# Kernel optimization log

Hardware: AMD Instinct MI355X
Metric: run time of the kernel (lower is better)

## Reference

```python
import jax, jax.numpy as jnp
import numpy as np
from jax import lax

NUM_HEADS = 8
RATIO_H = 2
RATIO_W = 2


def _layer_norm(x, gamma, beta, eps=1e-5):
    mean = jnp.mean(x, axis=-1, keepdims=True)
    var = jnp.var(x, axis=-1, keepdims=True)
    return (x - mean) * lax.rsqrt(var + eps) * gamma + beta


def setup_inputs() -> dict:
    key = jax.random.key(0)
    ks = jax.random.split(key, 6)
    B, N, C = 4, 4096, 512
    std = 0.02
    return {
        "x": jax.random.normal(ks[0], (B, N, C), jnp.float32),
        "w_qkv": jax.random.normal(ks[1], (3 * C, C), jnp.float32) * std,
        "w_ke": jax.random.normal(ks[2], (C, C, RATIO_H, RATIO_W), jnp.float32) * std,
        "w_ve": jax.random.normal(ks[3], (C, C, RATIO_H, RATIO_W), jnp.float32) * std,
        "gamma_k": jnp.ones((C // NUM_HEADS,), jnp.float32),
        "beta_k": jnp.zeros((C // NUM_HEADS,), jnp.float32),
        "gamma_v": jnp.ones((C // NUM_HEADS,), jnp.float32),
        "beta_v": jnp.zeros((C // NUM_HEADS,), jnp.float32),
        "w_proj": jax.random.normal(ks[4], (C, C), jnp.float32) * std,
        "b_proj": jnp.zeros((C,), jnp.float32),
    }


def reference(x, w_qkv, w_ke, w_ve, gamma_k, beta_k, gamma_v, beta_v, w_proj, b_proj):
    B, N, C = x.shape
    H = W = int(np.sqrt(N))
    h = NUM_HEADS
    hd = C // h
    s = RATIO_H * RATIO_W
    scale = hd ** -0.5

    # qkv projection (no bias): [B, N, 3C]
    qkv = jnp.einsum('bnc,dc->bnd', x, w_qkv)
    q, k, v = jnp.split(qkv, 3, axis=-1)

    # q -> [B, h, N, hd]
    q = q.reshape(B, N, h, hd).transpose(0, 2, 1, 3)

    # spatial reduction of k, v via strided conv (kernel == stride, no bias)
    def reduce_kv(t, w):
        img = t.transpose(0, 2, 1).reshape(B, C, H, W)
        red = lax.conv_general_dilated(
            img, w, window_strides=(RATIO_H, RATIO_W), padding='VALID',
            dimension_numbers=('NCHW', 'OIHW', 'NCHW'))  # [B, C, H/rh, W/rw]
        return red.reshape(B, C, N // s).transpose(0, 2, 1).reshape(
            B, N // s, h, hd).transpose(0, 2, 1, 3)  # [B, h, N/s, hd]

    k = _layer_norm(reduce_kv(k, w_ke), gamma_k, beta_k)
    v = _layer_norm(reduce_kv(v, w_ve), gamma_v, beta_v)

    # attention: [B, h, N, N/s]
    attn = jax.nn.softmax(jnp.einsum('bhqd,bhkd->bhqk', q, k) * scale, axis=-1)
    out = jnp.einsum('bhqk,bhkd->bhqd', attn, v)  # [B, h, N, hd]
    out = out.transpose(0, 2, 1, 3).reshape(B, N, C)
    return jnp.einsum('bnc,dc->bnd', out, w_proj) + b_proj
```

## Files before the change

### kernel.cpp

```cpp
#include <hip/hip_runtime.h>
#include <hip/hip_bf16.h>

#define DEVI static __device__ __forceinline__

typedef __attribute__((ext_vector_type(4))) float f32x4;
typedef __attribute__((ext_vector_type(8))) short bf16x8;
typedef __attribute__((ext_vector_type(4))) short s16x4;
typedef __attribute__((ext_vector_type(2))) unsigned int u32x2;

DEVI unsigned short f2bf(float f) {
    union { float f; unsigned u; } v; v.f = f;
    unsigned r = v.u + 0x7fffu + ((v.u >> 16) & 1u);
    return (unsigned short)(r >> 16);
}

DEVI void gload_lds16(const void* g, void* l) {
    __builtin_amdgcn_global_load_lds(
        (const __attribute__((address_space(1))) unsigned int*)(g),
        (__attribute__((address_space(3))) unsigned int*)(l), 16, 0, 0);
}

#define EXP2A(d, x) asm("v_exp_f32 %0, %1" : "=v"(d) : "v"(x))
#define CVTPK(d, a, b) asm("v_cvt_pk_bf16_f32 %0, %1, %2" : "=v"(d) : "v"(a), "v"(b))

__global__ __launch_bounds__(256) void prep_kernel(
    const float* __restrict__ x, const float* __restrict__ w_qkv,
    const float* __restrict__ w_proj, const float* __restrict__ w_ke,
    const float* __restrict__ w_ve,
    unsigned short* __restrict__ xb, unsigned short* __restrict__ wqkvb,
    unsigned short* __restrict__ wprojb, unsigned short* __restrict__ w2k,
    unsigned short* __restrict__ w2v, unsigned short* __restrict__ wqkvT)
{
    const int blk = blockIdx.x, t = threadIdx.x;
    if (blk < 9216) {
        const float* src; unsigned short* dst; int i;
        if (blk < 8192)      { src = x;      dst = xb;     i = (blk * 256 + t) * 4; }
        else if (blk < 8960) { src = w_qkv;  dst = wqkvb;  i = ((blk - 8192) * 256 + t) * 4; }
        else                 { src = w_proj; dst = wprojb; i = ((blk - 8960) * 256 + t) * 4; }
        const float4 v = *(const float4*)(src + i);
        ushort4 o; o.x = f2bf(v.x); o.y = f2bf(v.y); o.z = f2bf(v.z); o.w = f2bf(v.w);
        *(ushort4*)(dst + i) = o;
    } else if (blk < 11264) {
        const int r = blk - 9216;
        const float* wsrc = (r < 1024) ? w_ke : w_ve;
        unsigned short* wdst = (r < 1024) ? w2k : w2v;
        const int i4 = (((r & 1023) * 256) + t) * 4;
        const int o = i4 >> 11, p = (i4 >> 9) & 3, c = i4 & 511;
        const float* s = wsrc + (o << 11) + (c << 2) + p;
        ushort4 ov; ov.x = f2bf(s[0]); ov.y = f2bf(s[4]); ov.z = f2bf(s[8]); ov.w = f2bf(s[12]);
        *(ushort4*)(wdst + i4) = ov;
    } else {
        const int r2 = blk - 11264;
        const int i4 = (r2 * 256 + t) * 4;
        const int sel = i4 >> 18;
        const int rem = i4 & 262143;
        const int d = rem >> 9, c4 = rem & 511;
        const float* s = w_qkv + (size_t)(512 + sel * 512 + c4) * 512 + d;
        ushort4 ov; ov.x = f2bf(s[0]); ov.y = f2bf(s[512]); ov.z = f2bf(s[1024]); ov.w = f2bf(s[1536]);
        *(ushort4*)(wqkvT + i4) = ov;
    }
}

template<int OUT_BF16, int ADD_BIAS>
__global__ __launch_bounds__(256) void gemm_bt(
    const unsigned short* __restrict__ A,
    const unsigned short* __restrict__ B,
    void* __restrict__ Cp, const float* __restrict__ bias,
    int N, int K)
{
    __shared__ unsigned short As[128 * 64];
    __shared__ unsigned short Bs[128 * 64];
    const int t = threadIdx.x;
    const int lane = t & 63, w = t >> 6;
    const int wr = w >> 1, wc = w & 1;
    const int lr = lane & 15, lg = lane >> 4;
    const size_t rowBase = (size_t)blockIdx.y * 128;
    const size_t colBase = (size_t)blockIdx.x * 128;

    const unsigned short* gA[4]; const unsigned short* gB[4]; int du[4];
#pragma unroll
    for (int j = 0; j < 4; ++j) {
        const int u = t * 16 + j * 4096;
        const int row = u >> 7, colb = u & 127;
        const int csw = colb ^ ((row & 7) << 4);
        du[j] = u;
        gA[j] = A + (rowBase + row) * (size_t)K + (csw >> 1);
        gB[j] = B + (colBase + row) * (size_t)K + (csw >> 1);
    }
    const int sw = (lr & 7) << 4;

    f32x4 acc[4][4] = {};

    for (int k0 = 0; k0 < K; k0 += 64) {
#pragma unroll
        for (int j = 0; j < 4; ++j) {
            gload_lds16(gA[j] + k0, (char*)As + du[j]);
            gload_lds16(gB[j] + k0, (char*)Bs + du[j]);
        }
        __syncthreads();
#pragma unroll
        for (int s = 0; s < 2; ++s) {
            const int ro = (s * 64 + lg * 16) ^ sw;
            bf16x8 af[4], bfr[4];
#pragma unroll
            for (int a = 0; a < 4; ++a)
                af[a] = *(const bf16x8*)((char*)As + (wr * 64 + a * 16 + lr) * 128 + ro);
#pragma unroll
            for (int bn = 0; bn < 4; ++bn)
                bfr[bn] = *(const bf16x8*)((char*)Bs + (wc * 64 + bn * 16 + lr) * 128 + ro);
#pragma unroll
            for (int a = 0; a < 4; ++a)
#pragma unroll
                for (int bn = 0; bn < 4; ++bn)
                    acc[a][bn] = __builtin_amdgcn_mfma_f32_16x16x32_bf16(af[a], bfr[bn], acc[a][bn], 0, 0, 0);
        }
        __syncthreads();
    }

#pragma unroll
    for (int a = 0; a < 4; ++a) {
        const size_t row = rowBase + wr * 64 + a * 16 + lg * 4;
#pragma unroll
        for (int bn = 0; bn < 4; ++bn) {
            const size_t col = colBase + wc * 64 + bn * 16 + lr;
#pragma unroll
            for (int r = 0; r < 4; ++r) {
                const float v = acc[a][bn][r];
                if (OUT_BF16) {
                    ((unsigned short*)Cp)[(row + r) * (size_t)N + col] = f2bf(v);
                } else {
                    const float vb2 = ADD_BIAS ? (v + bias[col]) : v;
                    ((float*)Cp)[(row + r) * (size_t)N + col] = vb2;
                }
            }
        }
    }
}

__global__ __launch_bounds__(256) void gemm_wt(
    const unsigned short* __restrict__ w2k,
    const unsigned short* __restrict__ w2v,
    const unsigned short* __restrict__ wqkvT,
    unsigned short* __restrict__ wtk,
    unsigned short* __restrict__ wtv)
{
    __shared__ unsigned short As[128 * 64];
    __shared__ unsigned short Bs[128 * 64];
    const int t = threadIdx.x;
    const int lane = t & 63, w = t >> 6;
    const int wr = w >> 1, wc = w & 1;
    const int lr = lane & 15, lg = lane >> 4;
    const int rowBase = blockIdx.y * 128;
    const int colBase = blockIdx.x * 128;
    const int p = blockIdx.z & 3, sel = blockIdx.z >> 2;
    const unsigned short* A = (sel ? w2v : w2k) + p * 512;
    const unsigned short* B = wqkvT + (size_t)sel * 262144;
    unsigned short* C = (sel ? wtv : wtk) + p * 512;

    const unsigned short* gA[4]; const unsigned short* gB[4]; int du[4];
#pragma unroll
    for (int j = 0; j < 4; ++j) {
        const int u = t * 16 + j * 4096;
        const int row = u >> 7, colb = u & 127;
        const int csw = colb ^ ((row & 7) << 4);
        du[j] = u;
        gA[j] = A + (size_t)(rowBase + row) * 2048 + (csw >> 1);
        gB[j] = B + (size_t)(colBase + row) * 512 + (csw >> 1);
    }
    const int sw = (lr & 7) << 4;

    f32x4 acc[4][4] = {};

    for (int k0 = 0; k0 < 512; k0 += 64) {
#pragma unroll
        for (int j = 0; j < 4; ++j) {
            gload_lds16(gA[j] + k0, (char*)As + du[j]);
            gload_lds16(gB[j] + k0, (char*)Bs + du[j]);
        }
        __syncthreads();
#pragma unroll
        for (int s = 0; s < 2; ++s) {
            const int ro = (s * 64 + lg * 16) ^ sw;
            bf16x8 af[4], bfr[4];
#pragma unroll
            for (int a = 0; a < 4; ++a)
                af[a] = *(const bf16x8*)((char*)As + (wr * 64 + a * 16 + lr) * 128 + ro);
#pragma unroll
            for (int bn = 0; bn < 4; ++bn)
                bfr[bn] = *(const bf16x8*)((char*)Bs + (wc * 64 + bn * 16 + lr) * 128 + ro);
#pragma unroll
            for (int a = 0; a < 4; ++a)
#pragma unroll
                for (int bn = 0; bn < 4; ++bn)
                    acc[a][bn] = __builtin_amdgcn_mfma_f32_16x16x32_bf16(af[a], bfr[bn], acc[a][bn], 0, 0, 0);
        }
        __syncthreads();
    }

#pragma unroll
    for (int a = 0; a < 4; ++a) {
        const size_t row = (size_t)rowBase + wr * 64 + a * 16 + lg * 4;
#pragma unroll
        for (int bn = 0; bn < 4; ++bn) {
            const size_t col = (size_t)colBase + wc * 64 + bn * 16 + lr;
#pragma unroll
            for (int r = 0; r < 4; ++r)
                C[(row + r) * 2048 + col] = f2bf(acc[a][bn][r]);
        }
    }
}

__global__ __launch_bounds__(256) void gemm_red(
    const unsigned short* __restrict__ xb,
    const unsigned short* __restrict__ wtk,
    const unsigned short* __restrict__ wtv,
    float* __restrict__ kred)
{
    __shared__ unsigned short As[128 * 64];
    __shared__ unsigned short Bs[128 * 64];
    const int t = threadIdx.x;
    const int lane = t & 63, w = t >> 6;
    const int wr = w >> 1, wc = w & 1;
    const int lr = lane & 15, lg = lane >> 4;
    const int rowBase = blockIdx.y * 128;
    const int colBase = blockIdx.x * 128;
    const int ks = blockIdx.z;
    const int isV = rowBase >= 4096;
    const unsigned short* Bp = isV ? wtv : wtk;

    const char* gA[4]; const unsigned short* gB[4]; int du[4];
#pragma unroll
    for (int j = 0; j < 4; ++j) {
        const int u = t * 16 + j * 4096;
        const int row = u >> 7, colb = u & 127;
        const int csw = colb ^ ((row & 7) << 4);
        du[j] = u;
        const int bm = (rowBase + row) & 4095;
        const int b = bm >> 10, m = bm & 1023;
        const int pix = (m >> 5) * 128 + (m & 31) * 2;
        gA[j] = (const char*)xb + (size_t)(b * 4096 + pix) * 1024 + csw;
        gB[j] = Bp + (colBase + row) * (size_t)2048 + (csw >> 1);
    }
    const int sw = (lr & 7) << 4;

    f32x4 acc[4][4] = {};

    for (int kk = 0; kk < 16; ++kk) {
        const int k0 = ks * 1024 + kk * 64;
        const int p = k0 >> 9;
        const int pd = ((p & 1) ? 1 : 0) + ((p & 2) ? 64 : 0);
        const size_t aoff = (size_t)pd * 1024 + (size_t)(k0 & 511) * 2;
#pragma unroll
        for (int j = 0; j < 4; ++j) {
            gload_lds16(gA[j] + aoff, (char*)As + du[j]);
            gload_lds16(gB[j] + k0, (char*)Bs + du[j]);
        }
        __syncthreads();
#pragma unroll
        for (int s = 0; s < 2; ++s) {
            const int ro = (s * 64 + lg * 16) ^ sw;
            bf16x8 af[4], bfr[4];
#pragma unroll
            for (int a = 0; a < 4; ++a)
                af[a] = *(const bf16x8*)((char*)As + (wr * 64 + a * 16 + lr) * 128 + ro);
#pragma unroll
            for (int bn = 0; bn < 4; ++bn)
                bfr[bn] = *(const bf16x8*)((char*)Bs + (wc * 64 + bn * 16 + lr) * 128 + ro);
#pragma unroll
            for (int a = 0; a < 4; ++a)
#pragma unroll
                for (int bn = 0; bn < 4; ++bn)
                    acc[a][bn] = __builtin_amdgcn_mfma_f32_16x16x32_bf16(af[a], bfr[bn], acc[a][bn], 0, 0, 0);
        }
        __syncthreads();
    }

    float* outp = kred + (size_t)ks * 4194304;
#pragma unroll
    for (int a = 0; a < 4; ++a) {
        const size_t row = (size_t)rowBase + wr * 64 + a * 16 + lg * 4;
#pragma unroll
        for (int bn = 0; bn < 4; ++bn) {
            const size_t col = (size_t)colBase + wc * 64 + bn * 16 + lr;
#pragma unroll
            for (int r = 0; r < 4; ++r)
                outp[(row + r) * 512 + col] = acc[a][bn][r];
        }
    }
}

__global__ __launch_bounds__(256) void ln_kernel(
    const float* __restrict__ kredA, const float* __restrict__ kredB,
    const float* __restrict__ gk, const float* __restrict__ bk,
    const float* __restrict__ gv, const float* __restrict__ bv,
    unsigned short* __restrict__ outp)
{
    const int bm = blockIdx.x;
    const int sel = blockIdx.y;
    const size_t off = ((size_t)sel * 4096 + bm) * 512;
    const float* g = sel ? gv : gk;
    const float* be = sel ? bv : bk;
    const float QS = sel ? 1.0f : 0.18033688011112042f;
    unsigned short* o = outp + off;
    const int t = threadIdx.x;
    const float2 a = *(const float2*)(kredA + off + t * 2);
    const float2 b2 = *(const float2*)(kredB + off + t * 2);
    const float vx = a.x + b2.x, vy = a.y + b2.y;
    float s = vx + vy, s2 = vx * vx + vy * vy;
#pragma unroll
    for (int o2 = 1; o2 <= 16; o2 <<= 1) {
        s += __shfl_xor(s, o2);
        s2 += __shfl_xor(s2, o2);
    }
    const float mean = s * 0.015625f;
    const float var = s2 * 0.015625f - mean * mean;
    const float rstd = rsqrtf(var + 1e-5f);
    const int c = (t * 2) & 63;
    ushort2 ov;
    ov.x = f2bf(((vx - mean) * rstd * g[c] + be[c]) * QS);
    ov.y = f2bf(((vy - mean) * rstd * g[c + 1] + be[c + 1]) * QS);
    *(ushort2*)(o + t * 2) = ov;
}

__global__ __launch_bounds__(256) void transpose_v(
    const unsigned short* __restrict__ v_ln, unsigned short* __restrict__ v_t)
{
    __shared__ unsigned short tile[64][65];
    const int mb = blockIdx.x;
    const int cb = blockIdx.y;
    const int t = threadIdx.x;
#pragma unroll
    for (int i = 0; i < 16; ++i) {
        const int idx = i * 256 + t;
        const int r = idx >> 6, c = idx & 63;
        tile[r][c] = v_ln[(size_t)(mb * 64 + r) * 512 + cb * 64 + c];
    }
    __syncthreads();
    const int b = mb >> 4;
    const int mloc = (mb & 15) * 64;
#pragma unroll
    for (int i = 0; i < 16; ++i) {
        const int idx = i * 256 + t;
        const int c = idx >> 6, m = idx & 63;
        v_t[((size_t)(b * 512) + cb * 64 + c) * 1024 + mloc + m] = tile[m][c];
    }
}

__global__ __launch_bounds__(256) void attn_kernel(
    const unsigned short* __restrict__ qb,
    const unsigned short* __restrict__ k_ln,
    const unsigned short* __restrict__ v_t,
    unsigned short* __restrict__ attn_out)
{
    extern __shared__ char smem[];
    const int blk = ((blockIdx.x & 7) << 7) | (blockIdx.x >> 3);
    const int qc = blk & 31, h = (blk >> 5) & 7, b = blk >> 8;
    const int t = threadIdx.x, w = t >> 6, lane = t & 63;
    const int lr = lane & 15, lg = lane >> 4;
    const int qrow0 = qc * 128 + w * 32;

    const unsigned short* qpA = qb + (size_t)(b * 4096 + qrow0 + lr) * 512 + h * 64 + lg * 8;
    const bf16x8 qa0 = *(const bf16x8*)(qpA);
    const bf16x8 qa1 = *(const bf16x8*)(qpA + 32);
    const bf16x8 qb0 = *(const bf16x8*)(qpA + 16 * 512);
    const bf16x8 qb1 = *(const bf16x8*)(qpA + 16 * 512 + 32);

    const char* kbase = (const char*)(k_ln + (size_t)b * 524288 + h * 64);
    const char* vbase = (const char*)(v_t + ((size_t)b * 512 + h * 64) * 1024);
    const int d0 = t * 16, d1 = 4096 + t * 16;
    const int r0 = d0 >> 7, cs0 = (d0 & 127) ^ ((r0 & 7) << 4);
    const int r1 = d1 >> 7, cs1 = (d1 & 127) ^ ((r1 & 7) << 4);
    const char* gK0 = kbase + r0 * 1024 + cs0;
    const char* gK1 = kbase + r1 * 1024 + cs1;
    const char* gV0 = vbase + r0 * 2048 + cs0;
    const char* gV1 = vbase + r1 * 2048 + cs1;

#define STAGE_KV(buf, kt) do { \
    gload_lds16(gK0 + (size_t)(kt) * 65536, smem + (buf) * 8192 + d0); \
    gload_lds16(gK1 + (size_t)(kt) * 65536, smem + (buf) * 8192 + d1); \
    gload_lds16(gV0 + (kt) * 128, smem + 16384 + (buf) * 8192 + d0); \
    gload_lds16(gV1 + (kt) * 128, smem + 16384 + (buf) * 8192 + d1); \
  } while (0)

    bf16x8 ones;
#pragma unroll
    for (int i = 0; i < 8; ++i) ones[i] = (short)0x3F80;

    f32x4 accA[4] = {}, accB[4] = {};
    f32x4 psaccA = {}, psaccB = {};

    STAGE_KV(0, 0);
    __syncthreads();

    char* Pw = smem + 32768 + w * 2048;
    const int sw = (lr & 7) << 4;
    const int off0 = lr * 128 + ((lg * 16) ^ sw);
    const int off1 = lr * 128 + ((64 + lg * 16) ^ sw);
    int pwo[4];
#pragma unroll
    for (int tt = 0; tt < 4; ++tt) pwo[tt] = lr * 128 + ((tt * 32 + lg * 8) ^ sw);

#pragma unroll 2
    for (int kt = 0; kt < 16; ++kt) {
        const int cur = kt & 1;
        if (kt < 15) STAGE_KV(cur ^ 1, kt + 1);
        const char* KsB = smem + cur * 8192;
        const char* VsB = smem + 16384 + cur * 8192;

        f32x4 sa[4], sb[4];
#pragma unroll
        for (int tt = 0; tt < 4; ++tt) {
            const bf16x8 kf0 = *(const bf16x8*)(KsB + tt * 2048 + off0);
            const bf16x8 kf1 = *(const bf16x8*)(KsB + tt * 2048 + off1);
            f32x4 za = {}, zb = {};
            za = __builtin_amdgcn_mfma_f32_16x16x32_bf16(kf0, qa0, za, 0, 0, 0);
            za = __builtin_amdgcn_mfma_f32_16x16x32_bf16(kf1, qa1, za, 0, 0, 0);
            zb = __builtin_amdgcn_mfma_f32_16x16x32_bf16(kf0, qb0, zb, 0, 0, 0);
            zb = __builtin_amdgcn_mfma_f32_16x16x32_bf16(kf1, qb1, zb, 0, 0, 0);
            sa[tt] = za; sb[tt] = zb;
        }

#pragma unroll
        for (int tt = 0; tt < 4; ++tt) {
            float e0, e1, e2, e3;
            EXP2A(e0, sa[tt][0]); EXP2A(e1, sa[tt][1]);
            EXP2A(e2, sa[tt][2]); EXP2A(e3, sa[tt][3]);
            unsigned c0, c1;
            CVTPK(c0, e0, e1); CVTPK(c1, e2, e3);
            union { u32x2 u; s16x4 s; } pk; pk.u.x = c0; pk.u.y = c1;
            *(s16x4*)(Pw + pwo[tt]) = pk.s;
        }
        asm volatile("" ::: "memory");
        const bf16x8 fa0 = *(const bf16x8*)(Pw + off0);
        const bf16x8 fa1 = *(const bf16x8*)(Pw + off1);
        asm volatile("" ::: "memory");

        bf16x8 vf0[4], vf1[4];
#pragma unroll
        for (int n2 = 0; n2 < 4; ++n2) {
            vf0[n2] = *(const bf16x8*)(VsB + n2 * 2048 + off0);
            vf1[n2] = *(const bf16x8*)(VsB + n2 * 2048 + off1);
        }

#pragma unroll
        for (int n2 = 0; n2 < 4; ++n2) {
            accA[n2] = __builtin_amdgcn_mfma_f32_16x16x32_bf16(fa0, vf0[n2], accA[n2], 0, 0, 0);
            accA[n2] = __builtin_amdgcn_mfma_f32_16x16x32_bf16(fa1, vf1[n2], accA[n2], 0, 0, 0);
        }
        psaccA = __builtin_amdgcn_mfma_f32_16x16x32_bf16(fa0, ones, psaccA, 0, 0, 0);
        psaccA = __builtin_amdgcn_mfma_f32_16x16x32_bf16(fa1, ones, psaccA, 0, 0, 0);

#pragma unroll
        for (int tt = 0; tt < 4; ++tt) {
            float e0, e1, e2, e3;
            EXP2A(e0, sb[tt][0]); EXP2A(e1, sb[tt][1]);
            EXP2A(e2, sb[tt][2]); EXP2A(e3, sb[tt][3]);
            unsigned c0, c1;
            CVTPK(c0, e0, e1); CVTPK(c1, e2, e3);
            union { u32x2 u; s16x4 s; } pk; pk.u.x = c0; pk.u.y = c1;
            *(s16x4*)(Pw + pwo[tt]) = pk.s;
        }
        asm volatile("" ::: "memory");
        const bf16x8 fb0 = *(const bf16x8*)(Pw + off0);
        const bf16x8 fb1 = *(const bf16x8*)(Pw + off1);

#pragma unroll
        for (int n2 = 0; n2 < 4; ++n2) {
            accB[n2] = __builtin_amdgcn_mfma_f32_16x16x32_bf16(fb0, vf0[n2], accB[n2], 0, 0, 0);
            accB[n2] = __builtin_amdgcn_mfma_f32_16x16x32_bf16(fb1, vf1[n2], accB[n2], 0, 0, 0);
        }
        psaccB = __builtin_amdgcn_mfma_f32_16x16x32_bf16(fb0, ones, psaccB, 0, 0, 0);
        psaccB = __builtin_amdgcn_mfma_f32_16x16x32_bf16(fb1, ones, psaccB, 0, 0, 0);
        __syncthreads();
    }
#undef STAGE_KV

    float dA[4], dB[4];
#pragma unroll
    for (int r = 0; r < 4; ++r) {
        dA[r] = 1.0f / psaccA[r];
        dB[r] = 1.0f / psaccB[r];
    }
    unsigned short* oA = attn_out + (size_t)(b * 4096 + qrow0 + lg * 4) * 512 + h * 64;
#pragma unroll
    for (int n2 = 0; n2 < 4; ++n2)
#pragma unroll
        for (int r = 0; r < 4; ++r) {
            oA[(size_t)r * 512 + n2 * 16 + lr] = f2bf(accA[n2][r] * dA[r]);
            oA[(size_t)(16 + r) * 512 + n2 * 16 + lr] = f2bf(accB[n2][r] * dB[r]);
        }
}

extern "C" void kernel_launch(void* const* d_in, const int* in_sizes, int n_in,
                              void* d_out, int out_size, void* d_ws, size_t ws_size,
                              hipStream_t stream)
{
    (void)in_sizes; (void)n_in; (void)out_size; (void)ws_size;
    const float* x       = (const float*)d_in[0];
    const float* w_qkv   = (const float*)d_in[1];
    const float* w_ke    = (const float*)d_in[2];
    const float* w_ve    = (const float*)d_in[3];
    const float* gamma_k = (const float*)d_in[4];
    const float* beta_k  = (const float*)d_in[5];
    const float* gamma_v = (const float*)d_in[6];
    const float* beta_v  = (const float*)d_in[7];
    const float* w_proj  = (const float*)d_in[8];
    const float* b_proj  = (const float*)d_in[9];
    float* out = (float*)d_out;

    char* ws = (char*)d_ws;
    unsigned short* qb     = (unsigned short*)(ws + 0);
    unsigned short* wtk    = (unsigned short*)(ws + 16777216);
    unsigned short* wtv    = (unsigned short*)(ws + 18874368);
    unsigned short* wqkvT  = (unsigned short*)(ws + 20971520);
    unsigned short* xb     = (unsigned short*)(ws + 50331648);
    unsigned short* attn_o = xb;
    float*          kredB  = (float*)(ws + 67108864);
    float*          kredA  = (float*)(ws + 83886080);
    unsigned short* k_ln   = (unsigned short*)(ws + 100663296);
    unsigned short* v_ln   = (unsigned short*)(ws + 104857600);
    unsigned short* v_t    = (unsigned short*)(ws + 109051904);
    unsigned short* wqkvb  = (unsigned short*)(ws + 113246208);
    unsigned short* w2k    = (unsigned short*)(ws + 114819072);
    unsigned short* w2v    = (unsigned short*)(ws + 116916224);
    unsigned short* wprojb = (unsigned short*)(ws + 119013376);

    prep_kernel<<<11776, 256, 0, stream>>>(x, w_qkv, w_proj, w_ke, w_ve,
                                           xb, wqkvb, wprojb, w2k, w2v, wqkvT);

    gemm_wt<<<dim3(4, 4, 8), 256, 0, stream>>>(w2k, w2v, wqkvT, wtk, wtv);

    gemm_bt<1, 0><<<dim3(4, 128), 256, 0, stream>>>(
        xb, wqkvb, qb, nullptr, 512, 512);

    gemm_red<<<dim3(4, 64, 2), 256, 0, stream>>>(xb, wtk, wtv, kredB);

    ln_kernel<<<dim3(4096, 2), 256, 0, stream>>>(kredA, kredB,
                                                 gamma_k, beta_k, gamma_v, beta_v, k_ln);

    transpose_v<<<dim3(64, 8), 256, 0, stream>>>(v_ln, v_t);

    attn_kernel<<<1024, 256, 40960, stream>>>(qb, k_ln, v_t, attn_o);

    gemm_bt<0, 1><<<dim3(4, 128), 256, 0, stream>>>(
        attn_o, wprojb, out, b_proj, 512, 512);
}
```

Measured before the change: 145.4 us.

## Merge Q projection and KV reduction GEMMs into one launch; prioritize MFMA in attention

Combines the Q projection GEMM and the spatial-reduction K/V GEMM into a single kernel launch whose grid is split by blockIdx.y, so both workloads share the GPU concurrently and one launch plus its tail is removed. Also wraps the MFMA sections of the attention loop with s_setprio raising wave priority, to favor matrix-core issue over exp/convert phases of other waves. The merged kernel carries both code paths, which may raise register usage and lower occupancy.

```diff
diff --git a/kernel.cpp b/kernel.cpp
--- a/kernel.cpp
+++ b/kernel.cpp
@@ -210,8 +210,10 @@
     }
 }
 
-__global__ __launch_bounds__(256) void gemm_red(
+__global__ __launch_bounds__(256) void gemm_qred(
     const unsigned short* __restrict__ xb,
+    const unsigned short* __restrict__ wqkvb,
+    unsigned short* __restrict__ qbuf,
     const unsigned short* __restrict__ wtk,
     const unsigned short* __restrict__ wtv,
     float* __restrict__ kred)
@@ -222,69 +224,119 @@
     const int lane = t & 63, w = t >> 6;
     const int wr = w >> 1, wc = w & 1;
     const int lr = lane & 15, lg = lane >> 4;
-    const int rowBase = blockIdx.y * 128;
+    const int sw = (lr & 7) << 4;
     const int colBase = blockIdx.x * 128;
-    const int ks = blockIdx.z;
-    const int isV = rowBase >= 4096;
-    const unsigned short* Bp = isV ? wtv : wtk;
-
-    const char* gA[4]; const unsigned short* gB[4]; int du[4];
-#pragma unroll
-    for (int j = 0; j < 4; ++j) {
-        const int u = t * 16 + j * 4096;
-        const int row = u >> 7, colb = u & 127;
-        const int csw = colb ^ ((row & 7) << 4);
-        du[j] = u;
-        const int bm = (rowBase + row) & 4095;
-        const int b = bm >> 10, m = bm & 1023;
-        const int pix = (m >> 5) * 128 + (m & 31) * 2;
-        gA[j] = (const char*)xb + (size_t)(b * 4096 + pix) * 1024 + csw;
-        gB[j] = Bp + (colBase + row) * (size_t)2048 + (csw >> 1);
-    }
-    const int sw = (lr & 7) << 4;
-
-    f32x4 acc[4][4] = {};
-
-    for (int kk = 0; kk < 16; ++kk) {
-        const int k0 = ks * 1024 + kk * 64;
-        const int p = k0 >> 9;
-        const int pd = ((p & 1) ? 1 : 0) + ((p & 2) ? 64 : 0);
-        const size_t aoff = (size_t)pd * 1024 + (size_t)(k0 & 511) * 2;
+
+    if (blockIdx.y < 128) {
+        const size_t rowBase = (size_t)blockIdx.y * 128;
+        const unsigned short* gA[4]; const unsigned short* gB[4]; int du[4];
 #pragma unroll
         for (int j = 0; j < 4; ++j) {
-            gload_lds16(gA[j] + aoff, (char*)As + du[j]);
-            gload_lds16(gB[j] + k0, (char*)Bs + du[j]);
-        }
-        __syncthreads();
-#pragma unroll
-        for (int s = 0; s < 2; ++s) {
-            const int ro = (s * 64 + lg * 16) ^ sw;
-            bf16x8 af[4], bfr[4];
-#pragma unroll
-            for (int a = 0; a < 4; ++a)
-                af[a] = *(const bf16x8*)((char*)As + (wr * 64 + a * 16 + lr) * 128 + ro);
-#pragma unroll
-            for (int bn = 0; bn < 4; ++bn)
-                bfr[bn] = *(const bf16x8*)((char*)Bs + (wc * 64 + bn * 16 + lr) * 128 + ro);
-#pragma unroll
-            for (int a = 0; a < 4; ++a)
+            const int u = t * 16 + j * 4096;
+            const int row = u >> 7, colb = u & 127;
+            const int csw = colb ^ ((row & 7) << 4);
+            du[j] = u;
+            gA[j] = xb + (rowBase + row) * (size_t)512 + (csw >> 1);
+            gB[j] = wqkvb + (colBase + row) * (size_t)512 + (csw >> 1);
+        }
+        f32x4 acc[4][4] = {};
+        for (int k0 = 0; k0 < 512; k0 += 64) {
+#pragma unroll
+            for (int j = 0; j < 4; ++j) {
+                gload_lds16(gA[j] + k0, (char*)As + du[j]);
+                gload_lds16(gB[j] + k0, (char*)Bs + du[j]);
+            }
+            __syncthreads();
+#pragma unroll
+            for (int s = 0; s < 2; ++s) {
+                const int ro = (s * 64 + lg * 16) ^ sw;
+                bf16x8 af[4], bfr[4];
+#pragma unroll
+                for (int a = 0; a < 4; ++a)
+                    af[a] = *(const bf16x8*)((char*)As + (wr * 64 + a * 16 + lr) * 128 + ro);
 #pragma unroll
                 for (int bn = 0; bn < 4; ++bn)
-                    acc[a][bn] = __builtin_amdgcn_mfma_f32_16x16x32_bf16(af[a], bfr[bn], acc[a][bn], 0, 0, 0);
-        }
-        __syncthreads();
-    }
-
-    float* outp = kred + (size_t)ks * 4194304;
-#pragma unroll
-    for (int a = 0; a < 4; ++a) {
-        const size_t row = (size_t)rowBase + wr * 64 + a * 16 + lg * 4;
-#pragma unroll
-        for (int bn = 0; bn < 4; ++bn) {
-            const size_t col = (size_t)colBase + wc * 64 + bn * 16 + lr;
-#pragma unroll
-            for (int r = 0; r < 4; ++r)
-                outp[(row + r) * 512 + col] = acc[a][bn][r];
+                    bfr[bn] = *(const bf16x8*)((char*)Bs + (wc * 64 + bn * 16 + lr) * 128 + ro);
+#pragma unroll
+                for (int a = 0; a < 4; ++a)
+#pragma unroll
+                    for (int bn = 0; bn < 4; ++bn)
+                        acc[a][bn] = __builtin_amdgcn_mfma_f32_16x16x32_bf16(af[a], bfr[bn], acc[a][bn], 0, 0, 0);
+            }
+            __syncthreads();
+        }
+#pragma unroll
+        for (int a = 0; a < 4; ++a) {
+            const size_t row = rowBase + wr * 64 + a * 16 + lg * 4;
+#pragma unroll
+            for (int bn = 0; bn < 4; ++bn) {
+                const size_t col = (size_t)colBase + wc * 64 + bn * 16 + lr;
+#pragma unroll
+                for (int r = 0; r < 4; ++r)
+                    qbuf[(row + r) * 512 + col] = f2bf(acc[a][bn][r]);
+            }
+        }
+    } else {
+        const int z = blockIdx.y - 128;
+        const int ks = z >> 6;
+        const int rowBase = (z & 63) * 128;
+        const int isV = rowBase >= 4096;
+        const unsigned short* Bp = isV ? wtv : wtk;
+
+        const char* gA[4]; const unsigned short* gB[4]; int du[4];
+#pragma unroll
+        for (int j = 0; j < 4; ++j) {
+            const int u = t * 16 + j * 4096;
+            const int row = u >> 7, colb = u & 127;
+            const int csw = colb ^ ((row & 7) << 4);
+            du[j] = u;
+            const int bm = (rowBase + row) & 4095;
+            const int b = bm >> 10, m = bm & 1023;
+            const int pix = (m >> 5) * 128 + (m & 31) * 2;
+            gA[j] = (const char*)xb + (size_t)(b * 4096 + pix) * 1024 + csw;
+            gB[j] = Bp + (colBase + row) * (size_t)2048 + (csw >> 1);
+        }
+        f32x4 acc[4][4] = {};
+        for (int kk = 0; kk < 16; ++kk) {
+            const int k0 = ks * 1024 + kk * 64;
+            const int p = k0 >> 9;
+            const int pd = ((p & 1) ? 1 : 0) + ((p & 2) ? 64 : 0);
+            const size_t aoff = (size_t)pd * 1024 + (size_t)(k0 & 511) * 2;
+#pragma unroll
+            for (int j = 0; j < 4; ++j) {
+                gload_lds16(gA[j] + aoff, (char*)As + du[j]);
+                gload_lds16(gB[j] + k0, (char*)Bs + du[j]);
+            }
+            __syncthreads();
+#pragma unroll
+            for (int s = 0; s < 2; ++s) {
+                const int ro = (s * 64 + lg * 16) ^ sw;
+                bf16x8 af[4], bfr[4];
+#pragma unroll
+                for (int a = 0; a < 4; ++a)
+                    af[a] = *(const bf16x8*)((char*)As + (wr * 64 + a * 16 + lr) * 128 + ro);
+#pragma unroll
+                for (int bn = 0; bn < 4; ++bn)
+                    bfr[bn] = *(const bf16x8*)((char*)Bs + (wc * 64 + bn * 16 + lr) * 128 + ro);
+#pragma unroll
+                for (int a = 0; a < 4; ++a)
+#pragma unroll
+                    for (int bn = 0; bn < 4; ++bn)
+                        acc[a][bn] = __builtin_amdgcn_mfma_f32_16x16x32_bf16(af[a], bfr[bn], acc[a][bn], 0, 0, 0);
+            }
+            __syncthreads();
+        }
+        float* outp = kred + (size_t)ks * 4194304;
+#pragma unroll
+        for (int a = 0; a < 4; ++a) {
+            const size_t row = (size_t)rowBase + wr * 64 + a * 16 + lg * 4;
+#pragma unroll
+            for (int bn = 0; bn < 4; ++bn) {
+                const size_t col = (size_t)colBase + wc * 64 + bn * 16 + lr;
+#pragma unroll
+                for (int r = 0; r < 4; ++r)
+                    outp[(row + r) * 512 + col] = acc[a][bn][r];
+            }
         }
     }
 }
@@ -408,6 +460,7 @@
         const char* VsB = smem + 16384 + cur * 8192;
 
         f32x4 sa[4], sb[4];
+        __builtin_amdgcn_s_setprio(1);
 #pragma unroll
         for (int tt = 0; tt < 4; ++tt) {
             const bf16x8 kf0 = *(const bf16x8*)(KsB + tt * 2048 + off0);
@@ -419,6 +472,7 @@
             zb = __builtin_amdgcn_mfma_f32_16x16x32_bf16(kf1, qb1, zb, 0, 0, 0);
             sa[tt] = za; sb[tt] = zb;
         }
+        __builtin_amdgcn_s_setprio(0);
 
 #pragma unroll
         for (int tt = 0; tt < 4; ++tt) {
@@ -442,6 +496,7 @@
             vf1[n2] = *(const bf16x8*)(VsB + n2 * 2048 + off1);
         }
 
+        __builtin_amdgcn_s_setprio(1);
 #pragma unroll
         for (int n2 = 0; n2 < 4; ++n2) {
             accA[n2] = __builtin_amdgcn_mfma_f32_16x16x32_bf16(fa0, vf0[n2], accA[n2], 0, 0, 0);
@@ -449,6 +504,7 @@
         }
         psaccA = __builtin_amdgcn_mfma_f32_16x16x32_bf16(fa0, ones, psaccA, 0, 0, 0);
         psaccA = __builtin_amdgcn_mfma_f32_16x16x32_bf16(fa1, ones, psaccA, 0, 0, 0);
+        __builtin_amdgcn_s_setprio(0);
 
 #pragma unroll
         for (int tt = 0; tt < 4; ++tt) {
@@ -464,6 +520,7 @@
         const bf16x8 fb0 = *(const bf16x8*)(Pw + off0);
         const bf16x8 fb1 = *(const bf16x8*)(Pw + off1);
 
+        __builtin_amdgcn_s_setprio(1);
 #pragma unroll
         for (int n2 = 0; n2 < 4; ++n2) {
             accB[n2] = __builtin_amdgcn_mfma_f32_16x16x32_bf16(fb0, vf0[n2], accB[n2], 0, 0, 0);
@@ -471,6 +528,7 @@
         }
         psaccB = __builtin_amdgcn_mfma_f32_16x16x32_bf16(fb0, ones, psaccB, 0, 0, 0);
         psaccB = __builtin_amdgcn_mfma_f32_16x16x32_bf16(fb1, ones, psaccB, 0, 0, 0);
+        __builtin_amdgcn_s_setprio(0);
         __syncthreads();
     }
 #undef STAGE_KV
@@ -530,10 +588,7 @@
 
     gemm_wt<<<dim3(4, 4, 8), 256, 0, stream>>>(w2k, w2v, wqkvT, wtk, wtv);
 
-    gemm_bt<1, 0><<<dim3(4, 128), 256, 0, stream>>>(
-        xb, wqkvb, qb, nullptr, 512, 512);
-
-    gemm_red<<<dim3(4, 64, 2), 256, 0, stream>>>(xb, wtk, wtv, kredB);
+    gemm_qred<<<dim3(4, 256), 256, 0, stream>>>(xb, wqkvb, qb, wtk, wtv, kredB);
 
     ln_kernel<<<dim3(4096, 2), 256, 0, stream>>>(kredA, kredB,
                                                  gamma_k, beta_k, gamma_v, beta_v, k_ln);
```

New measurement: 143.8 us. Within noise of the previous version (-1.1%).
